# Kernel tuning notes

Measured on AMD Instinct MI355X. Metric: run time of the kernel, lower is better.

The kernel has to match this reference:

```python
import jax, jax.numpy as jnp
import numpy as np

N = 16384
C = 128
F = 128

def setup_inputs() -> dict:
    key = jax.random.key(0)
    k1, k2, k3, k4 = jax.random.split(key, 4)
    X = jax.random.normal(k1, (N, C), dtype=jnp.float32)
    adj = jax.random.uniform(k2, (N, N), dtype=jnp.float32)
    W = jax.random.normal(k3, (C, F), dtype=jnp.float32) * 0.05
    b = jax.random.normal(k4, (F,), dtype=jnp.float32) * 0.05
    return {"X": X, "adj": adj, "W": W, "b": b}

def reference(X, adj, W, b):
    # adj_hat = adj + I (self-loops)
    adj_hat = adj + jnp.eye(adj.shape[0], dtype=adj.dtype)
    # D^{-1/2}: inverse of sqrt of the diagonal degree matrix == 1/sqrt(rowsum)
    d_inv_sqrt = 1.0 / jnp.sqrt(jnp.sum(adj_hat, axis=1))  # [N]
    # Symmetric normalization via row/col scaling (same math as D^-1/2 @ A @ D^-1/2)
    adj_norm = adj_hat * d_inv_sqrt[:, None] * d_inv_sqrt[None, :]
    # Feature transform first (N*C*F) then aggregate (N*N*F)
    out = adj_norm @ (X @ W) + b
    return jax.nn.relu(out)
```

## Files before the change

### kernel.cpp

```cpp
#include <hip/hip_runtime.h>
#include <hip/hip_bf16.h>

typedef __attribute__((ext_vector_type(8))) short short8;
typedef __attribute__((ext_vector_type(4))) float f32x4;

#define N_NODES 16384
#define FEAT 128
#define NTILES 256
#define KSPLIT 2
#define NT2 (NTILES / KSPLIT)

__device__ __forceinline__ short f2bf(float x) {
  union { float f; unsigned u; } v;
  v.f = x;
  unsigned r = v.u + 0x7fffu + ((v.u >> 16) & 1u);
  return (short)(r >> 16);
}

__global__ __launch_bounds__(256) void rowsum_kernel(
    const float* __restrict__ adj, float* __restrict__ dinv)
{
  const int row = blockIdx.x;
  const float4* p4 = (const float4*)(adj + (size_t)row * N_NODES);
  float s = 0.f;
  #pragma unroll 4
  for (int i = threadIdx.x; i < N_NODES / 4; i += 256) {
    float4 v = p4[i];
    s += (v.x + v.y) + (v.z + v.w);
  }
  #pragma unroll
  for (int off = 32; off > 0; off >>= 1) s += __shfl_down(s, off, 64);
  __shared__ float part[4];
  if ((threadIdx.x & 63) == 0) part[threadIdx.x >> 6] = s;
  __syncthreads();
  if (threadIdx.x == 0) {
    float tot = (part[0] + part[1]) + (part[2] + part[3]) + 1.0f;
    dinv[row] = rsqrtf(tot);
  }
}

__global__ __launch_bounds__(256) void xw_kernel(
    const float* __restrict__ X, const float* __restrict__ W,
    const float* __restrict__ dinv,
    __hip_bfloat16* __restrict__ Ypack)
{
  __shared__ __align__(16) float Ws[64][128];
  __shared__ __align__(16) float Xs[32][128];
  __shared__ __align__(16) short Ts[128][40];
  const int tid = threadIdx.x;
  const int row0 = blockIdx.x << 5;

  {
    const float4* Xg = (const float4*)(X + ((size_t)row0 << 7));
    float4* Xl = (float4*)&Xs[0][0];
    #pragma unroll
    for (int i = 0; i < 4; ++i) Xl[tid + (i << 8)] = Xg[tid + (i << 8)];
  }
  const int f  = tid & 127;
  const int rr = tid >> 7;
  float acc[16];
  #pragma unroll
  for (int k = 0; k < 16; ++k) acc[k] = 0.f;

  for (int cc = 0; cc < 2; ++cc) {
    __syncthreads();
    {
      const float4* Wg = (const float4*)(W + ((size_t)cc << 13));
      float4* Wl = (float4*)&Ws[0][0];
      #pragma unroll
      for (int i = 0; i < 8; ++i) Wl[tid + (i << 8)] = Wg[tid + (i << 8)];
    }
    __syncthreads();
    for (int c4 = 0; c4 < 16; ++c4) {
      const int cl = c4 << 2;
      const float w0 = Ws[cl + 0][f];
      const float w1 = Ws[cl + 1][f];
      const float w2 = Ws[cl + 2][f];
      const float w3 = Ws[cl + 3][f];
      const int cg = (cc << 6) + cl;
      #pragma unroll
      for (int k = 0; k < 16; ++k) {
        const float4 x = *(const float4*)&Xs[rr + (k << 1)][cg];
        acc[k] += x.x * w0 + x.y * w1 + x.z * w2 + x.w * w3;
      }
    }
  }
  #pragma unroll
  for (int k = 0; k < 16; ++k) {
    const int r = rr + (k << 1);
    const float dv = dinv[row0 + r];
    Ts[f][r] = f2bf(acc[k] * dv);
  }
  __syncthreads();
  {
    const int f2 = tid >> 1;
    const int h  = (tid & 1) << 4;
    const short8 v0 = *(const short8*)&Ts[f2][h];
    const short8 v1 = *(const short8*)&Ts[f2][h + 8];
    short* o = (short*)Ypack;
    *(short8*)(o + (size_t)(row0 + h) * FEAT + (f2 << 3))     = v0;
    *(short8*)(o + (size_t)(row0 + h + 8) * FEAT + (f2 << 3)) = v1;
  }
}

__global__ __launch_bounds__(1024, 4) void spmm_kernel(
    const float* __restrict__ A,
    const __hip_bfloat16* __restrict__ Ypack,
    float* __restrict__ pws)
{
  __shared__ __align__(16) short As[2][8192];
  __shared__ __align__(16) short Bs[3][8192];

  const int tid = threadIdx.x;
  const int rb  = blockIdx.x;
  const int lb  = ((rb & 7) << 5) | (rb >> 3);
  const int mt  = lb & 127;
  const int s   = lb >> 7;
  const int row0 = mt << 7;

  const int ar  = tid >> 3;
  const int akg = tid & 7;
  const float* Ag = A + (size_t)(row0 + ar) * N_NODES + (s * NT2 << 6) + (akg << 3);
  const short* Yg = (const short*)Ypack + ((size_t)(s * NT2) << 13) + (tid << 3);

  const int wid  = tid >> 6;
  const int wm   = wid >> 1;
  const int wf   = wid & 1;
  const int lane = tid & 63;
  const int lm   = lane & 15;
  const int lkg  = lane >> 4;
  const int myrow = (wm << 4) + lm;

  f32x4 acc[4];
  #pragma unroll
  for (int c = 0; c < 4; ++c) acc[c] = (f32x4){0.f, 0.f, 0.f, 0.f};

  float4 a0A, a1A, a0B, a1B;

#define GLDSY(T, P)                                                            \
  {                                                                            \
    const short* ys_ = Yg + ((size_t)(T) << 13);                               \
    __builtin_amdgcn_global_load_lds(                                          \
        (const __attribute__((address_space(1))) void*)ys_,                    \
        (__attribute__((address_space(3))) void*)&Bs[P][wid << 9], 16, 0, 0);  \
  }

#define LOADA(T, A0_, A1_)                                                     \
  {                                                                            \
    const float* ap = Ag + ((size_t)(T) << 6);                                 \
    A0_ = *(const float4*)(ap);                                                \
    A1_ = *(const float4*)(ap + 4);                                            \
  }

#define STORA(T, P, A0_, A1_)                                                  \
  {                                                                            \
    const int j = (row0 + ar) - ((s * NT2 + (T)) << 6) - (akg << 3);           \
    if (j >= 0 && j < 8) {                                  \
      A0_.x += (j == 0) ? 1.f : 0.f;  A0_.y += (j == 1) ? 1.f : 0.f;           \
      A0_.z += (j == 2) ? 1.f : 0.f;  A0_.w += (j == 3) ? 1.f : 0.f;           \
      A1_.x += (j == 4) ? 1.f : 0.f;  A1_.y += (j == 5) ? 1.f : 0.f;           \
      A1_.z += (j == 6) ? 1.f : 0.f;  A1_.w += (j == 7) ? 1.f : 0.f;           \
    }                                                                          \
    short8 av;                                                                 \
    av[0] = f2bf(A0_.x); av[1] = f2bf(A0_.y); av[2] = f2bf(A0_.z);             \
    av[3] = f2bf(A0_.w); av[4] = f2bf(A1_.x); av[5] = f2bf(A1_.y);             \
    av[6] = f2bf(A1_.z); av[7] = f2bf(A1_.w);                                  \
    *(short8*)&As[P][(akg << 10) + (ar << 3)] = av;                            \
  }

#define COMP(AP, BP)                                                           \
  {                                                                            \
    const short8 af0 = *(const short8*)&As[AP][(lkg << 10) + (myrow << 3)];    \
    acc[0] = __builtin_amdgcn_mfma_f32_16x16x32_bf16(af0,                      \
        *(const short8*)&Bs[BP][(lkg << 10) + (((wf << 6) + lm) << 3)], acc[0], 0, 0, 0); \
    acc[1] = __builtin_amdgcn_mfma_f32_16x16x32_bf16(af0,                      \
        *(const short8*)&Bs[BP][(lkg << 10) + (((wf << 6) + 16 + lm) << 3)], acc[1], 0, 0, 0); \
    acc[2] = __builtin_amdgcn_mfma_f32_16x16x32_bf16(af0,                      \
        *(const short8*)&Bs[BP][(lkg << 10) + (((wf << 6) + 32 + lm) << 3)], acc[2], 0, 0, 0); \
    acc[3] = __builtin_amdgcn_mfma_f32_16x16x32_bf16(af0,                      \
        *(const short8*)&Bs[BP][(lkg << 10) + (((wf << 6) + 48 + lm) << 3)], acc[3], 0, 0, 0); \
    const short8 af1 = *(const short8*)&As[AP][((4 + lkg) << 10) + (myrow << 3)]; \
    acc[0] = __builtin_amdgcn_mfma_f32_16x16x32_bf16(af1,                      \
        *(const short8*)&Bs[BP][((4 + lkg) << 10) + (((wf << 6) + lm) << 3)], acc[0], 0, 0, 0); \
    acc[1] = __builtin_amdgcn_mfma_f32_16x16x32_bf16(af1,                      \
        *(const short8*)&Bs[BP][((4 + lkg) << 10) + (((wf << 6) + 16 + lm) << 3)], acc[1], 0, 0, 0); \
    acc[2] = __builtin_amdgcn_mfma_f32_16x16x32_bf16(af1,                      \
        *(const short8*)&Bs[BP][((4 + lkg) << 10) + (((wf << 6) + 32 + lm) << 3)], acc[2], 0, 0, 0); \
    acc[3] = __builtin_amdgcn_mfma_f32_16x16x32_bf16(af1,                      \
        *(const short8*)&Bs[BP][((4 + lkg) << 10) + (((wf << 6) + 48 + lm) << 3)], acc[3], 0, 0, 0); \
  }

  GLDSY(0, 0)
  LOADA(0, a0A, a1A)
  GLDSY(1, 1)
  LOADA(1, a0B, a1B)
  STORA(0, 0, a0A, a1A)
  asm volatile("s_waitcnt lgkmcnt(0)" ::: "memory");
  __builtin_amdgcn_s_barrier();

  int bp = 0;
  for (int t = 0; t < NT2; t += 2) {
    int bw = bp + 2; if (bw >= 3) bw -= 3;
    if (t + 2 < NT2) { GLDSY(t + 2, bw) LOADA(t + 2, a0A, a1A) }
    __builtin_amdgcn_s_setprio(1);
    COMP(0, bp)
    __builtin_amdgcn_s_setprio(0);
    if (t + 1 < NT2) STORA(t + 1, 1, a0B, a1B)
    if (t + 2 < NT2) { asm volatile("s_waitcnt vmcnt(3)" ::: "memory"); }
    else             { asm volatile("s_waitcnt vmcnt(0)" ::: "memory"); }
    asm volatile("s_waitcnt lgkmcnt(0)" ::: "memory");
    __builtin_amdgcn_s_barrier();
    int bp1 = bp + 1; if (bp1 >= 3) bp1 -= 3;
    int bw1 = bp1 + 2; if (bw1 >= 3) bw1 -= 3;
    if (t + 3 < NT2) { GLDSY(t + 3, bw1) LOADA(t + 3, a0B, a1B) }
    __builtin_amdgcn_s_setprio(1);
    COMP(1, bp1)
    __builtin_amdgcn_s_setprio(0);
    if (t + 2 < NT2) STORA(t + 2, 0, a0A, a1A)
    if (t + 3 < NT2) { asm volatile("s_waitcnt vmcnt(3)" ::: "memory"); }
    else             { asm volatile("s_waitcnt vmcnt(0)" ::: "memory"); }
    asm volatile("s_waitcnt lgkmcnt(0)" ::: "memory");
    __builtin_amdgcn_s_barrier();
    bp = bp1 + 1; if (bp >= 3) bp -= 3;
  }

  float* pp = pws + ((size_t)(s * N_NODES + row0)) * FEAT;
  const int lr = (lane >> 4) << 2;
  #pragma unroll
  for (int c = 0; c < 4; ++c) {
    const int col = (wf << 6) + (c << 4) + lm;
    #pragma unroll
    for (int r = 0; r < 4; ++r) {
      pp[(size_t)((wm << 4) + lr + r) * FEAT + col] = acc[c][r];
    }
  }
#undef GLDSY
#undef LOADA
#undef STORA
#undef COMP
}

__global__ __launch_bounds__(256) void reduce_kernel(
    const float* __restrict__ pws, const float* __restrict__ dinv,
    const float* __restrict__ bias, float* __restrict__ out)
{
  const int idx4 = blockIdx.x * 256 + threadIdx.x;
  const int row  = idx4 >> 5;
  const int f4   = idx4 & 31;
  const float4 p0 = ((const float4*)pws)[idx4];
  const float4 p1 = ((const float4*)pws)[idx4 + (N_NODES * FEAT / 4)];
  const float4 bv = ((const float4*)bias)[f4];
  const float  d  = dinv[row];
  float4 v;
  v.x = d * (p0.x + p1.x) + bv.x;
  v.y = d * (p0.y + p1.y) + bv.y;
  v.z = d * (p0.z + p1.z) + bv.z;
  v.w = d * (p0.w + p1.w) + bv.w;
  v.x = v.x > 0.f ? v.x : 0.f;
  v.y = v.y > 0.f ? v.y : 0.f;
  v.z = v.z > 0.f ? v.z : 0.f;
  v.w = v.w > 0.f ? v.w : 0.f;
  ((float4*)out)[idx4] = v;
}

extern "C" void kernel_launch(void* const* d_in, const int* in_sizes, int n_in,
                              void* d_out, int out_size, void* d_ws, size_t ws_size,
                              hipStream_t stream) {
  const float* X   = (const float*)d_in[0];
  const float* adj = (const float*)d_in[1];
  const float* W   = (const float*)d_in[2];
  const float* b   = (const float*)d_in[3];
  float* out = (float*)d_out;

  float* dinv           = (float*)d_ws;
  __hip_bfloat16* Ypack = (__hip_bfloat16*)((char*)d_ws + (1 << 16));
  float* pws            = (float*)((char*)d_ws + (1 << 16) + (1 << 22));

  rowsum_kernel<<<N_NODES, 256, 0, stream>>>(adj, dinv);
  xw_kernel<<<N_NODES / 32, 256, 0, stream>>>(X, W, dinv, Ypack);
  spmm_kernel<<<128 * KSPLIT, 1024, 0, stream>>>(adj, Ypack, pws);
  reduce_kernel<<<N_NODES * FEAT / 4 / 256, 256, 0, stream>>>(pws, dinv, b, out);
}
```

Baseline: 416.2 us.

## Double K tile to 128 and switch spmm pipeline to simple double buffering

```diff
diff --git a/kernel.cpp b/kernel.cpp
--- a/kernel.cpp
+++ b/kernel.cpp
@@ -6,9 +6,8 @@
 
 #define N_NODES 16384
 #define FEAT 128
-#define NTILES 256
 #define KSPLIT 2
-#define NT2 (NTILES / KSPLIT)
+#define NT2 64
 
 __device__ __forceinline__ short f2bf(float x) {
   union { float f; unsigned u; } v;
@@ -108,8 +107,8 @@
     const __hip_bfloat16* __restrict__ Ypack,
     float* __restrict__ pws)
 {
-  __shared__ __align__(16) short As[2][8192];
-  __shared__ __align__(16) short Bs[3][8192];
+  __shared__ __align__(16) short As[2][16384];
+  __shared__ __align__(16) short Bs[2][16384];
 
   const int tid = threadIdx.x;
   const int rb  = blockIdx.x;
@@ -118,10 +117,10 @@
   const int s   = lb >> 7;
   const int row0 = mt << 7;
 
-  const int ar  = tid >> 3;
-  const int akg = tid & 7;
-  const float* Ag = A + (size_t)(row0 + ar) * N_NODES + (s * NT2 << 6) + (akg << 3);
-  const short* Yg = (const short*)Ypack + ((size_t)(s * NT2) << 13) + (tid << 3);
+  const int ar = tid >> 3;
+  const int kg = tid & 7;
+  const float* Ag = A + (size_t)(row0 + ar) * N_NODES + (s << 13) + (kg << 4);
+  const short* Yg = (const short*)Ypack + ((size_t)s << 20) + (tid << 3);
 
   const int wid  = tid >> 6;
   const int wm   = wid >> 1;
@@ -135,93 +134,86 @@
   #pragma unroll
   for (int c = 0; c < 4; ++c) acc[c] = (f32x4){0.f, 0.f, 0.f, 0.f};
 
-  float4 a0A, a1A, a0B, a1B;
+  float4 pa0, pa1, pa2, pa3;
+
+#define LOADA(T)                                                               \
+  {                                                                            \
+    const float* ap = Ag + ((size_t)(T) << 7);                                 \
+    pa0 = *(const float4*)(ap);                                                \
+    pa1 = *(const float4*)(ap + 4);                                            \
+    pa2 = *(const float4*)(ap + 8);                                            \
+    pa3 = *(const float4*)(ap + 12);                                           \
+  }
 
 #define GLDSY(T, P)                                                            \
   {                                                                            \
-    const short* ys_ = Yg + ((size_t)(T) << 13);                               \
+    const short* ys_ = Yg + ((size_t)(T) << 14);                               \
     __builtin_amdgcn_global_load_lds(                                          \
         (const __attribute__((address_space(1))) void*)ys_,                    \
         (__attribute__((address_space(3))) void*)&Bs[P][wid << 9], 16, 0, 0);  \
-  }
-
-#define LOADA(T, A0_, A1_)                                                     \
-  {                                                                            \
-    const float* ap = Ag + ((size_t)(T) << 6);                                 \
-    A0_ = *(const float4*)(ap);                                                \
-    A1_ = *(const float4*)(ap + 4);                                            \
-  }
-
-#define STORA(T, P, A0_, A1_)                                                  \
-  {                                                                            \
-    const int j = (row0 + ar) - ((s * NT2 + (T)) << 6) - (akg << 3);           \
-    if (j >= 0 && j < 8) {                                  \
-      A0_.x += (j == 0) ? 1.f : 0.f;  A0_.y += (j == 1) ? 1.f : 0.f;           \
-      A0_.z += (j == 2) ? 1.f : 0.f;  A0_.w += (j == 3) ? 1.f : 0.f;           \
-      A1_.x += (j == 4) ? 1.f : 0.f;  A1_.y += (j == 5) ? 1.f : 0.f;           \
-      A1_.z += (j == 6) ? 1.f : 0.f;  A1_.w += (j == 7) ? 1.f : 0.f;           \
+    __builtin_amdgcn_global_load_lds(                                          \
+        (const __attribute__((address_space(1))) void*)(ys_ + 8192),           \
+        (__attribute__((address_space(3))) void*)&Bs[P][8192 + (wid << 9)],    \
+        16, 0, 0);                                                             \
+  }
+
+#define STORA(T, P)                                                            \
+  {                                                                            \
+    const int j = (row0 + ar) - (((s << 6) + (T)) << 7) - (kg << 4);           \
+    if (j >= 0 && j < 16) {                                 \
+      pa0.x += (j == 0)  ? 1.f : 0.f;  pa0.y += (j == 1)  ? 1.f : 0.f;         \
+      pa0.z += (j == 2)  ? 1.f : 0.f;  pa0.w += (j == 3)  ? 1.f : 0.f;         \
+      pa1.x += (j == 4)  ? 1.f : 0.f;  pa1.y += (j == 5)  ? 1.f : 0.f;         \
+      pa1.z += (j == 6)  ? 1.f : 0.f;  pa1.w += (j == 7)  ? 1.f : 0.f;         \
+      pa2.x += (j == 8)  ? 1.f : 0.f;  pa2.y += (j == 9)  ? 1.f : 0.f;         \
+      pa2.z += (j == 10) ? 1.f : 0.f;  pa2.w += (j == 11) ? 1.f : 0.f;         \
+      pa3.x += (j == 12) ? 1.f : 0.f;  pa3.y += (j == 13) ? 1.f : 0.f;         \
+      pa3.z += (j == 14) ? 1.f : 0.f;  pa3.w += (j == 15) ? 1.f : 0.f;         \
     }                                                                          \
-    short8 av;                                                                 \
-    av[0] = f2bf(A0_.x); av[1] = f2bf(A0_.y); av[2] = f2bf(A0_.z);             \
-    av[3] = f2bf(A0_.w); av[4] = f2bf(A1_.x); av[5] = f2bf(A1_.y);             \
-    av[6] = f2bf(A1_.z); av[7] = f2bf(A1_.w);                                  \
-    *(short8*)&As[P][(akg << 10) + (ar << 3)] = av;                            \
-  }
-
-#define COMP(AP, BP)                                                           \
-  {                                                                            \
-    const short8 af0 = *(const short8*)&As[AP][(lkg << 10) + (myrow << 3)];    \
-    acc[0] = __builtin_amdgcn_mfma_f32_16x16x32_bf16(af0,                      \
-        *(const short8*)&Bs[BP][(lkg << 10) + (((wf << 6) + lm) << 3)], acc[0], 0, 0, 0); \
-    acc[1] = __builtin_amdgcn_mfma_f32_16x16x32_bf16(af0,                      \
-        *(const short8*)&Bs[BP][(lkg << 10) + (((wf << 6) + 16 + lm) << 3)], acc[1], 0, 0, 0); \
-    acc[2] = __builtin_amdgcn_mfma_f32_16x16x32_bf16(af0,                      \
-        *(const short8*)&Bs[BP][(lkg << 10) + (((wf << 6) + 32 + lm) << 3)], acc[2], 0, 0, 0); \
-    acc[3] = __builtin_amdgcn_mfma_f32_16x16x32_bf16(af0,                      \
-        *(const short8*)&Bs[BP][(lkg << 10) + (((wf << 6) + 48 + lm) << 3)], acc[3], 0, 0, 0); \
-    const short8 af1 = *(const short8*)&As[AP][((4 + lkg) << 10) + (myrow << 3)]; \
-    acc[0] = __builtin_amdgcn_mfma_f32_16x16x32_bf16(af1,                      \
-        *(const short8*)&Bs[BP][((4 + lkg) << 10) + (((wf << 6) + lm) << 3)], acc[0], 0, 0, 0); \
-    acc[1] = __builtin_amdgcn_mfma_f32_16x16x32_bf16(af1,                      \
-        *(const short8*)&Bs[BP][((4 + lkg) << 10) + (((wf << 6) + 16 + lm) << 3)], acc[1], 0, 0, 0); \
-    acc[2] = __builtin_amdgcn_mfma_f32_16x16x32_bf16(af1,                      \
-        *(const short8*)&Bs[BP][((4 + lkg) << 10) + (((wf << 6) + 32 + lm) << 3)], acc[2], 0, 0, 0); \
-    acc[3] = __builtin_amdgcn_mfma_f32_16x16x32_bf16(af1,                      \
-        *(const short8*)&Bs[BP][((4 + lkg) << 10) + (((wf << 6) + 48 + lm) << 3)], acc[3], 0, 0, 0); \
-  }
-
+    short8 av0, av1;                                                           \
+    av0[0] = f2bf(pa0.x); av0[1] = f2bf(pa0.y); av0[2] = f2bf(pa0.z);          \
+    av0[3] = f2bf(pa0.w); av0[4] = f2bf(pa1.x); av0[5] = f2bf(pa1.y);          \
+    av0[6] = f2bf(pa1.z); av0[7] = f2bf(pa1.w);                                \
+    av1[0] = f2bf(pa2.x); av1[1] = f2bf(pa2.y); av1[2] = f2bf(pa2.z);          \
+    av1[3] = f2bf(pa2.w); av1[4] = f2bf(pa3.x); av1[5] = f2bf(pa3.y);          \
+    av1[6] = f2bf(pa3.z); av1[7] = f2bf(pa3.w);                                \
+    *(short8*)&As[P][((kg << 1) << 10) + (ar << 3)]       = av0;               \
+    *(short8*)&As[P][(((kg << 1) + 1) << 10) + (ar << 3)] = av1;               \
+  }
+
+#define COMP(P)                                                                \
+  {                                                                            \
+    _Pragma("unroll")                                                          \
+    for (int ks = 0; ks < 4; ++ks) {                                           \
+      const short8 af =                                                        \
+          *(const short8*)&As[P][(((ks << 2) + lkg) << 10) + (myrow << 3)];    \
+      _Pragma("unroll")                                                        \
+      for (int c = 0; c < 4; ++c) {                                            \
+        acc[c] = __builtin_amdgcn_mfma_f32_16x16x32_bf16(af,                   \
+            *(const short8*)&Bs[P][(((ks << 2) + lkg) << 10) +                 \
+                                   (((wf << 6) + (c << 4) + lm) << 3)],        \
+            acc[c], 0, 0, 0);                                                  \
+      }                                                                        \
+    }                                                                          \
+  }
+
+  LOADA(0)
   GLDSY(0, 0)
-  LOADA(0, a0A, a1A)
-  GLDSY(1, 1)
-  LOADA(1, a0B, a1B)
-  STORA(0, 0, a0A, a1A)
+  STORA(0, 0)
+  asm volatile("s_waitcnt vmcnt(0)" ::: "memory");
   asm volatile("s_waitcnt lgkmcnt(0)" ::: "memory");
   __builtin_amdgcn_s_barrier();
 
-  int bp = 0;
-  for (int t = 0; t < NT2; t += 2) {
-    int bw = bp + 2; if (bw >= 3) bw -= 3;
-    if (t + 2 < NT2) { GLDSY(t + 2, bw) LOADA(t + 2, a0A, a1A) }
+  for (int t = 0; t < NT2; ++t) {
+    const int p = t & 1;
+    if (t + 1 < NT2) { LOADA(t + 1) GLDSY(t + 1, p ^ 1) }
     __builtin_amdgcn_s_setprio(1);
-    COMP(0, bp)
+    COMP(p)
     __builtin_amdgcn_s_setprio(0);
-    if (t + 1 < NT2) STORA(t + 1, 1, a0B, a1B)
-    if (t + 2 < NT2) { asm volatile("s_waitcnt vmcnt(3)" ::: "memory"); }
-    else             { asm volatile("s_waitcnt vmcnt(0)" ::: "memory"); }
+    if (t + 1 < NT2) STORA(t + 1, p ^ 1)
+    asm volatile("s_waitcnt vmcnt(0)" ::: "memory");
     asm volatile("s_waitcnt lgkmcnt(0)" ::: "memory");
     __builtin_amdgcn_s_barrier();
-    int bp1 = bp + 1; if (bp1 >= 3) bp1 -= 3;
-    int bw1 = bp1 + 2; if (bw1 >= 3) bw1 -= 3;
-    if (t + 3 < NT2) { GLDSY(t + 3, bw1) LOADA(t + 3, a0B, a1B) }
-    __builtin_amdgcn_s_setprio(1);
-    COMP(1, bp1)
-    __builtin_amdgcn_s_setprio(0);
-    if (t + 2 < NT2) STORA(t + 2, 0, a0A, a1A)
-    if (t + 3 < NT2) { asm volatile("s_waitcnt vmcnt(3)" ::: "memory"); }
-    else             { asm volatile("s_waitcnt vmcnt(0)" ::: "memory"); }
-    asm volatile("s_waitcnt lgkmcnt(0)" ::: "memory");
-    __builtin_amdgcn_s_barrier();
-    bp = bp1 + 1; if (bp >= 3) bp -= 3;
   }
 
   float* pp = pws + ((size_t)(s * N_NODES + row0)) * FEAT;
@@ -234,8 +226,8 @@
       pp[(size_t)((wm << 4) + lr + r) * FEAT + col] = acc[c][r];
     }
   }
+#undef LOADA
 #undef GLDSY
-#undef LOADA
 #undef STORA
 #undef COMP
 }
```

Result: slower. 433.1 us (+4.0%).
